# Kernel tuning notes

Measured on AMD Instinct MI355X. Metric: run time of the kernel, lower is better.

## Reference

```python
import jax, jax.numpy as jnp
import numpy as np

N = 50000       # nodes
E = 800000      # random edges (self-loops appended in reference)
F_IN = 3        # dataset.num_features
CH = 32         # conv_hidden_channels
HEADS = 4       # attention_heads
C1_OUT = CH * 2     # 64
C2_OUT = CH * 4     # 128
LIN = 256       # lin_hidden_channels
NCLS = 25       # dataset.num_classes


def setup_inputs() -> dict:
    key = jax.random.key(0)
    ks = jax.random.split(key, 20)
    g = lambda k, s: (jax.random.normal(k, s, jnp.float32) * 0.05)
    return {
        "x": jax.random.normal(ks[0], (N, F_IN), jnp.float32),
        "edge_index": jax.random.randint(ks[1], (2, E), 0, N, dtype=jnp.int64),
        # fc0 (Linear stored as [in, out])
        "fc0_w": g(ks[2], (F_IN, CH)), "fc0_b": g(ks[3], (CH,)),
        # FeaStConv 1: in=CH, out=C1_OUT
        "conv1_w": g(ks[4], (CH, HEADS * C1_OUT)),
        "conv1_u": g(ks[5], (CH, HEADS)),
        "conv1_c": g(ks[6], (HEADS,)),
        "conv1_b": g(ks[7], (C1_OUT,)),
        # FeaStConv 2: in=C1_OUT, out=C2_OUT
        "conv2_w": g(ks[8], (C1_OUT, HEADS * C2_OUT)),
        "conv2_u": g(ks[9], (C1_OUT, HEADS)),
        "conv2_c": g(ks[10], (HEADS,)),
        "conv2_b": g(ks[11], (C2_OUT,)),
        # fc1, fc2
        "fc1_w": g(ks[12], (C2_OUT, LIN)), "fc1_b": g(ks[13], (LIN,)),
        "fc2_w": g(ks[14], (LIN, NCLS)), "fc2_b": g(ks[15], (NCLS,)),
    }


def feast_conv(x, src, dst, W, u, c, b):
    """FeaStConv (PyG): q = softmax((x_j - x_i) u + c) over heads,
    msg = sum_h q_h * (x_j W_h), mean-aggregated onto dst nodes."""
    xi = x[dst]                          # [E', in]
    xj = x[src]                          # [E', in]
    q = jax.nn.softmax((xj - xi) @ u + c, axis=-1)   # [E', H]
    m = (xj @ W).reshape(xj.shape[0], HEADS, -1)     # [E', H, out]
    msg = jnp.einsum('eh,ehd->ed', q, m)             # [E', out]
    agg = jax.ops.segment_sum(msg, dst, num_segments=N)
    cnt = jax.ops.segment_sum(jnp.ones((msg.shape[0],), x.dtype), dst,
                              num_segments=N)
    return agg / cnt[:, None] + b


def reference(x, edge_index, fc0_w, fc0_b,
              conv1_w, conv1_u, conv1_c, conv1_b,
              conv2_w, conv2_u, conv2_c, conv2_b,
              fc1_w, fc1_b, fc2_w, fc2_b):
    loops = jnp.arange(N, dtype=edge_index.dtype)
    src = jnp.concatenate([edge_index[0], loops])   # messages flow src -> dst
    dst = jnp.concatenate([edge_index[1], loops])
    h = jax.nn.elu(x @ fc0_w + fc0_b)
    h = jax.nn.elu(feast_conv(h, src, dst, conv1_w, conv1_u, conv1_c, conv1_b))
    h = jax.nn.elu(feast_conv(h, src, dst, conv2_w, conv2_u, conv2_c, conv2_b))
    h = jax.nn.elu(h @ fc1_w + fc1_b)
    # dropout skipped (eval mode / training=self.training)
    out = h @ fc2_w + fc2_b
    return jax.nn.log_softmax(out, axis=1)
```

## Files before the change

kernel.cpp:

```cpp
#include <hip/hip_runtime.h>
#include <math.h>

#define F_IN 3
#define CH 32
#define HEADS 4
#define C1_OUT 64
#define C2_OUT 128
#define LIN 256
#define NCLS 25
#define NBIN 8

typedef __attribute__((ext_vector_type(8))) short bf16x8;
typedef __attribute__((ext_vector_type(4))) float f32x4;

__device__ __forceinline__ float elu_f(float x) {
    return x > 0.f ? x : (__expf(x) - 1.f);
}

__device__ __forceinline__ unsigned short f2bf(float f) {
    union { float f; unsigned int u; } v; v.f = f;
    unsigned int u = v.u + 0x7fffu + ((v.u >> 16) & 1u);
    return (unsigned short)(u >> 16);
}

__device__ __forceinline__ float bf2f(unsigned short u) {
    union { unsigned int u; float f; } v; v.u = ((unsigned int)u) << 16;
    return v.f;
}

__device__ __forceinline__ void unpackq(uint2 qp, float& x, float& y,
                                        float& z, float& w) {
    x = bf2f((unsigned short)(qp.x & 0xffffu));
    y = bf2f((unsigned short)(qp.x >> 16));
    z = bf2f((unsigned short)(qp.y & 0xffffu));
    w = bf2f((unsigned short)(qp.y >> 16));
}

__device__ __forceinline__ void softmax4(const float* __restrict__ c,
                                         float& q0, float& q1, float& q2, float& q3) {
    float c0 = c[0], c1 = c[1], c2 = c[2], c3 = c[3];
    float mx = fmaxf(fmaxf(c0, c1), fmaxf(c2, c3));
    float e0 = __expf(c0 - mx), e1 = __expf(c1 - mx);
    float e2 = __expf(c2 - mx), e3 = __expf(c3 - mx);
    float inv = 1.f / (e0 + e1 + e2 + e3);
    q0 = e0 * inv; q1 = e1 * inv; q2 = e2 * inv; q3 = e3 * inv;
}

__global__ void k_fc0(const float* __restrict__ x, const float* __restrict__ w,
                      const float* __restrict__ b, unsigned short* __restrict__ h0,
                      int n_nodes) {
    int gid = blockIdx.x * blockDim.x + threadIdx.x;
    if (gid >= n_nodes * CH) return;
    int n = gid >> 5, c = gid & 31;
    float acc = b[c];
#pragma unroll
    for (int i = 0; i < F_IN; ++i) acc += x[n * F_IN + i] * w[i * CH + c];
    h0[gid] = f2bf(elu_f(acc));
}

__global__ void k_deg(const int* __restrict__ dst, int* __restrict__ deg,
                      int ne, int npb) {
    int bin = blockIdx.x & (NBIN - 1);
    int blk = blockIdx.x >> 3;
    int nblk = gridDim.x >> 3;
    int per = (ne + nblk - 1) / nblk;
    int start = blk * per;
    int end = start + per < ne ? start + per : ne;
    int lo = bin * npb, hi = lo + npb;
    for (int e = start + threadIdx.x; e < end; e += blockDim.x) {
        int d = dst[e];
        if (d >= lo && d < hi) atomicAdd(&deg[d], 1);
    }
}

#define SCAN_BS 1024
__global__ __launch_bounds__(SCAN_BS) void k_scan_a(
    const int* __restrict__ deg, int* __restrict__ offa,
    int* __restrict__ blksum, int n) {
    __shared__ int buf[SCAN_BS];
    int tid = threadIdx.x;
    int i = blockIdx.x * SCAN_BS + tid;
    int v = (i < n) ? deg[i] : 0;
    buf[tid] = v;
    __syncthreads();
    for (int s = 1; s < SCAN_BS; s <<= 1) {
        int t = (tid >= s) ? buf[tid - s] : 0;
        __syncthreads();
        buf[tid] += t;
        __syncthreads();
    }
    if (i < n) offa[i] = buf[tid] - v;
    if (tid == SCAN_BS - 1) blksum[blockIdx.x] = buf[tid];
}

__global__ void k_scan_b(int* __restrict__ blksum, int* __restrict__ offa,
                         int nblk, int n) {
    int tid = threadIdx.x;
    int orig = (tid < nblk) ? blksum[tid] : 0;
    int v = orig;
#pragma unroll
    for (int s = 1; s < 64; s <<= 1) {
        int t = __shfl_up(v, s, 64);
        if (tid >= s) v += t;
    }
    if (tid < nblk) blksum[tid] = v - orig;
    if (tid == nblk - 1) offa[n] = v;
}

__global__ void k_scan_c(int* __restrict__ offa, int* __restrict__ cur,
                         const int* __restrict__ blksum, int n) {
    int i = blockIdx.x * blockDim.x + threadIdx.x;
    if (i < n) {
        int o = offa[i] + blksum[i >> 10];
        offa[i] = o;
        cur[i] = o;
    }
}

__global__ void k_scatter(const int* __restrict__ eidx, int* __restrict__ cur,
                          int2* __restrict__ ssd, const float* __restrict__ p,
                          const float* __restrict__ cvec, uint2* __restrict__ qq,
                          int ne, int npb) {
    int bin = blockIdx.x & (NBIN - 1);
    int blk = blockIdx.x >> 3;
    int nblk = gridDim.x >> 3;
    int per = (ne + nblk - 1) / nblk;
    int start = blk * per;
    int end = start + per < ne ? start + per : ne;
    int lo = bin * npb, hi = lo + npb;
    float c0 = cvec[0], c1 = cvec[1], c2 = cvec[2], c3 = cvec[3];
    const float4* pp = (const float4*)p;
    for (int e = start + threadIdx.x; e < end; e += blockDim.x) {
        int d = eidx[ne + e];
        if (d >= lo && d < hi) {
            int s = eidx[e];
            int pos = atomicAdd(&cur[d], 1);
            ssd[pos] = make_int2(s, d);
            float4 ps = pp[s], pd = pp[d];
            float t0 = ps.x - pd.x + c0;
            float t1 = ps.y - pd.y + c1;
            float t2 = ps.z - pd.z + c2;
            float t3 = ps.w - pd.w + c3;
            float mx = fmaxf(fmaxf(t0, t1), fmaxf(t2, t3));
            float e0 = __expf(t0 - mx), e1 = __expf(t1 - mx);
            float e2 = __expf(t2 - mx), e3 = __expf(t3 - mx);
            float inv = 1.f / (e0 + e1 + e2 + e3);
            qq[pos] = make_uint2(
                (unsigned)f2bf(e0 * inv) | ((unsigned)f2bf(e1 * inv) << 16),
                (unsigned)f2bf(e2 * inv) | ((unsigned)f2bf(e3 * inv) << 16));
        }
    }
}

template<int IN>
__global__ void k_proj(const unsigned short* __restrict__ h,
                       const float* __restrict__ u,
                       float* __restrict__ p, int n_nodes) {
    int node = blockIdx.x * blockDim.x + threadIdx.x;
    if (node >= n_nodes) return;
    const unsigned short* hr = h + (size_t)node * IN;
    float a0 = 0.f, a1 = 0.f, a2 = 0.f, a3 = 0.f;
#pragma unroll
    for (int kb = 0; kb < IN; kb += 8) {
        uint4 uu = *(const uint4*)(hr + kb);
        unsigned int ws_[4] = {uu.x, uu.y, uu.z, uu.w};
#pragma unroll
        for (int j = 0; j < 4; ++j) {
            float vlo = bf2f((unsigned short)(ws_[j] & 0xffffu));
            float vhi = bf2f((unsigned short)(ws_[j] >> 16));
            int k0 = kb + j * 2, k1 = kb + j * 2 + 1;
            a0 = fmaf(vlo, u[k0 * HEADS + 0], a0); a0 = fmaf(vhi, u[k1 * HEADS + 0], a0);
            a1 = fmaf(vlo, u[k0 * HEADS + 1], a1); a1 = fmaf(vhi, u[k1 * HEADS + 1], a1);
            a2 = fmaf(vlo, u[k0 * HEADS + 2], a2); a2 = fmaf(vhi, u[k1 * HEADS + 2], a2);
            a3 = fmaf(vlo, u[k0 * HEADS + 3], a3); a3 = fmaf(vhi, u[k1 * HEADS + 3], a3);
        }
    }
    p[node * 4 + 0] = a0; p[node * 4 + 1] = a1;
    p[node * 4 + 2] = a2; p[node * 4 + 3] = a3;
}

__global__ void k_q(const float* __restrict__ p, const float* __restrict__ cvec,
                    const int2* __restrict__ ssd, uint2* __restrict__ qq, int ne) {
    int e = blockIdx.x * blockDim.x + threadIdx.x;
    if (e >= ne) return;
    int2 sd = ssd[e];
    const float4* pp = (const float4*)p;
    float4 ps = pp[sd.x], pd = pp[sd.y];
    float t0 = ps.x - pd.x + cvec[0];
    float t1 = ps.y - pd.y + cvec[1];
    float t2 = ps.z - pd.z + cvec[2];
    float t3 = ps.w - pd.w + cvec[3];
    float mx = fmaxf(fmaxf(t0, t1), fmaxf(t2, t3));
    float e0 = __expf(t0 - mx), e1 = __expf(t1 - mx);
    float e2 = __expf(t2 - mx), e3 = __expf(t3 - mx);
    float inv = 1.f / (e0 + e1 + e2 + e3);
    qq[e] = make_uint2(
        (unsigned)f2bf(e0 * inv) | ((unsigned)f2bf(e1 * inv) << 16),
        (unsigned)f2bf(e2 * inv) | ((unsigned)f2bf(e3 * inv) << 16));
}

__global__ __launch_bounds__(256) void k_agg1(
    const unsigned short* __restrict__ h, const int* __restrict__ offa,
    const int2* __restrict__ ssd, const uint2* __restrict__ qq,
    const float* __restrict__ cvec, unsigned short* __restrict__ arow,
    int n_nodes) {
    int wid = (blockIdx.x * blockDim.x + threadIdx.x) >> 6;
    int lane = threadIdx.x & 63;
    if (wid >= n_nodes) return;
    int half = lane >> 5, k = lane & 31;
    int e0 = offa[wid], e1 = offa[wid + 1];
    float a0 = 0.f, a1 = 0.f, a2 = 0.f, a3 = 0.f;
    for (int e = e0 + half; e < e1; e += 8) {
        int s[4]; uint2 qp[4]; float xv[4];
#pragma unroll
        for (int j = 0; j < 4; ++j) {
            int ee = e + 2 * j;
            int ec = ee < e1 ? ee : e0;
            s[j] = ssd[ec].x;
            uint2 q = qq[ec];
            if (ee >= e1) { q.x = 0u; q.y = 0u; }
            qp[j] = q;
        }
#pragma unroll
        for (int j = 0; j < 4; ++j) xv[j] = bf2f(h[(size_t)s[j] * CH + k]);
#pragma unroll
        for (int j = 0; j < 4; ++j) {
            float qx, qy, qz, qw;
            unpackq(qp[j], qx, qy, qz, qw);
            a0 = fmaf(qx, xv[j], a0); a1 = fmaf(qy, xv[j], a1);
            a2 = fmaf(qz, xv[j], a2); a3 = fmaf(qw, xv[j], a3);
        }
    }
    a0 += __shfl_xor(a0, 32); a1 += __shfl_xor(a1, 32);
    a2 += __shfl_xor(a2, 32); a3 += __shfl_xor(a3, 32);
    if (half == 0) {
        float qc0, qc1, qc2, qc3;
        softmax4(cvec, qc0, qc1, qc2, qc3);
        float xi = bf2f(h[(size_t)wid * CH + k]);
        a0 = fmaf(qc0, xi, a0); a1 = fmaf(qc1, xi, a1);
        a2 = fmaf(qc2, xi, a2); a3 = fmaf(qc3, xi, a3);
        float inv = 1.f / (float)(e1 - e0 + 1);
        arow[(size_t)wid * 128 + 0 * CH + k] = f2bf(a0 * inv);
        arow[(size_t)wid * 128 + 1 * CH + k] = f2bf(a1 * inv);
        arow[(size_t)wid * 128 + 2 * CH + k] = f2bf(a2 * inv);
        arow[(size_t)wid * 128 + 3 * CH + k] = f2bf(a3 * inv);
    }
}

__global__ __launch_bounds__(256) void k_agg2(
    const unsigned short* __restrict__ h, const int* __restrict__ offa,
    const int2* __restrict__ ssd, const uint2* __restrict__ qq,
    const float* __restrict__ cvec, unsigned short* __restrict__ arow,
    int n_nodes) {
    int wid = (blockIdx.x * blockDim.x + threadIdx.x) >> 6;
    int lane = threadIdx.x & 63;
    if (wid >= n_nodes) return;
    int e0 = offa[wid], e1 = offa[wid + 1];
    float a0 = 0.f, a1 = 0.f, a2 = 0.f, a3 = 0.f;
    for (int e = e0; e < e1; e += 8) {
        int s[8]; uint2 qp[8]; float xv[8];
#pragma unroll
        for (int j = 0; j < 8; ++j) {
            int ee = e + j;
            int ec = ee < e1 ? ee : e0;
            s[j] = ssd[ec].x;
            uint2 q = qq[ec];
            if (ee >= e1) { q.x = 0u; q.y = 0u; }
            qp[j] = q;
        }
#pragma unroll
        for (int j = 0; j < 8; ++j) xv[j] = bf2f(h[(size_t)s[j] * C1_OUT + lane]);
#pragma unroll
        for (int j = 0; j < 8; ++j) {
            float qx, qy, qz, qw;
            unpackq(qp[j], qx, qy, qz, qw);
            a0 = fmaf(qx, xv[j], a0); a1 = fmaf(qy, xv[j], a1);
            a2 = fmaf(qz, xv[j], a2); a3 = fmaf(qw, xv[j], a3);
        }
    }
    float qc0, qc1, qc2, qc3;
    softmax4(cvec, qc0, qc1, qc2, qc3);
    float xi = bf2f(h[(size_t)wid * C1_OUT + lane]);
    a0 = fmaf(qc0, xi, a0); a1 = fmaf(qc1, xi, a1);
    a2 = fmaf(qc2, xi, a2); a3 = fmaf(qc3, xi, a3);
    float inv = 1.f / (float)(e1 - e0 + 1);
    arow[(size_t)wid * 256 + 0 * C1_OUT + lane] = f2bf(a0 * inv);
    arow[(size_t)wid * 256 + 1 * C1_OUT + lane] = f2bf(a1 * inv);
    arow[(size_t)wid * 256 + 2 * C1_OUT + lane] = f2bf(a2 * inv);
    arow[(size_t)wid * 256 + 3 * C1_OUT + lane] = f2bf(a3 * inv);
}

template<int K, int M, int IN>
__global__ void k_prepB(const float* __restrict__ W, unsigned short* __restrict__ Bt) {
    int idx = blockIdx.x * blockDim.x + threadIdx.x;
    if (idx >= K * M) return;
    int o = idx / K, j = idx % K;
    float v;
    if (IN > 0) {
        int hh = j / IN, k = j % IN;
        v = W[k * (HEADS * M) + hh * M + o];
    } else {
        v = W[j * M + o];
    }
    Bt[idx] = f2bf(v);
}

__global__ void k_prepC(const float* __restrict__ W, unsigned short* __restrict__ Bt) {
    int idx = blockIdx.x * blockDim.x + threadIdx.x;
    if (idx >= 32 * LIN) return;
    int o = idx >> 8, k = idx & 255;
    float v = (o < NCLS) ? W[k * NCLS + o] : 0.f;
    Bt[o * LIN + k] = f2bf(v);
}

template<int K, int M>
__global__ __launch_bounds__(256) void k_mgemm(
    const unsigned short* __restrict__ A, const unsigned short* __restrict__ Bt,
    const float* __restrict__ bias, unsigned short* __restrict__ D, int n) {
    constexpr int CPW = M / 4;
    constexpr int NCF = CPW / 16;
    constexpr int NKC = K / 32;
    __shared__ unsigned short Al[64 * K];
    int tid = threadIdx.x;
    int w = tid >> 6, l = tid & 63;
    int l16 = l & 15, l4 = l >> 4;
    int rowbase = blockIdx.x * 64;

    bf16x8 bfr[NCF][NKC];
#pragma unroll
    for (int c = 0; c < NCF; ++c)
#pragma unroll
        for (int t = 0; t < NKC; ++t) {
            int col = w * CPW + c * 16 + l16;
            int k = t * 32 + l4 * 8;
            bfr[c][t] = *(const bf16x8*)(Bt + (size_t)col * K + k);
        }

    constexpr int CHUNKS = 64 * K / 8;
    for (int idx = tid; idx < CHUNKS; idx += 256) {
        int row = idx / (K / 8);
        int kb = (idx % (K / 8)) * 8;
        int grow = rowbase + row;
        uint4 u;
        if (grow < n) u = *(const uint4*)(A + (size_t)grow * K + kb);
        else          u.x = u.y = u.z = u.w = 0u;
        int byte = ((row * K + kb) * 2) ^ ((row & 7) << 4);
        *(uint4*)((char*)Al + byte) = u;
    }
    __syncthreads();

#pragma unroll
    for (int r = 0; r < 4; ++r) {
        bf16x8 af[NKC];
        int row = r * 16 + l16;
#pragma unroll
        for (int t = 0; t < NKC; ++t) {
            int byte = ((row * K + t * 32 + l4 * 8) * 2) ^ ((row & 7) << 4);
            af[t] = *(bf16x8*)((char*)Al + byte);
        }
#pragma unroll
        for (int c = 0; c < NCF; ++c) {
            f32x4 acc = {0.f, 0.f, 0.f, 0.f};
#pragma unroll
            for (int t = 0; t < NKC; ++t)
                acc = __builtin_amdgcn_mfma_f32_16x16x32_bf16(af[t], bfr[c][t], acc, 0, 0, 0);
            int col = w * CPW + c * 16 + l16;
            float bv = bias[col];
#pragma unroll
            for (int j = 0; j < 4; ++j) {
                int grow = rowbase + r * 16 + l4 * 4 + j;
                if (grow < n)
                    D[(size_t)grow * M + col] = f2bf(elu_f(acc[j] + bv));
            }
        }
    }
}

__global__ __launch_bounds__(256) void k_fc2m(
    const unsigned short* __restrict__ A, const unsigned short* __restrict__ Bt,
    const float* __restrict__ bias, float* __restrict__ out, int n) {
    int tid = threadIdx.x;
    int w = tid >> 6, l = tid & 63;
    int l16 = l & 15, l4 = l >> 4;
    int rowbase = blockIdx.x * 256 + w * 64;

    bf16x8 bfr0[8], bfr1[8];
#pragma unroll
    for (int t = 0; t < 8; ++t) {
        int k = t * 32 + l4 * 8;
        bfr0[t] = *(const bf16x8*)(Bt + (size_t)l16 * LIN + k);
        bfr1[t] = *(const bf16x8*)(Bt + (size_t)(16 + l16) * LIN + k);
    }
    float b0 = bias[l16];
    bool hi_ok = (l16 < NCLS - 16);
    float b1 = hi_ok ? bias[16 + l16] : 0.f;

#pragma unroll
    for (int r = 0; r < 4; ++r) {
        int arow_i = rowbase + r * 16 + l16;
        int arc = arow_i < n ? arow_i : n - 1;
        const unsigned short* ar = A + (size_t)arc * LIN;
        bf16x8 af[8];
#pragma unroll
        for (int t = 0; t < 8; ++t)
            af[t] = *(const bf16x8*)(ar + t * 32 + l4 * 8);
        f32x4 acc0 = {0.f, 0.f, 0.f, 0.f}, acc1 = {0.f, 0.f, 0.f, 0.f};
#pragma unroll
        for (int t = 0; t < 8; ++t) {
            acc0 = __builtin_amdgcn_mfma_f32_16x16x32_bf16(af[t], bfr0[t], acc0, 0, 0, 0);
            acc1 = __builtin_amdgcn_mfma_f32_16x16x32_bf16(af[t], bfr1[t], acc1, 0, 0, 0);
        }
#pragma unroll
        for (int j = 0; j < 4; ++j) {
            float v0 = acc0[j] + b0;
            float v1 = acc1[j] + b1;
            float m = fmaxf(v0, hi_ok ? v1 : -1e30f);
#pragma unroll
            for (int msk = 8; msk >= 1; msk >>= 1)
                m = fmaxf(m, __shfl_xor(m, msk, 16));
            float s = __expf(v0 - m) + (hi_ok ? __expf(v1 - m) : 0.f);
#pragma unroll
            for (int msk = 8; msk >= 1; msk >>= 1)
                s += __shfl_xor(s, msk, 16);
            float lse = m + __logf(s);
            int ro = rowbase + r * 16 + l4 * 4 + j;
            if (ro < n) {
                out[(size_t)ro * NCLS + l16] = v0 - lse;
                if (hi_ok) out[(size_t)ro * NCLS + 16 + l16] = v1 - lse;
            }
        }
    }
}

extern "C" void kernel_launch(void* const* d_in, const int* in_sizes, int n_in,
                              void* d_out, int out_size, void* d_ws, size_t ws_size,
                              hipStream_t stream) {
    const float* x     = (const float*)d_in[0];
    const int*   eidx  = (const int*)d_in[1];
    const float* fc0_w = (const float*)d_in[2];
    const float* fc0_b = (const float*)d_in[3];
    const float* c1w   = (const float*)d_in[4];
    const float* c1u   = (const float*)d_in[5];
    const float* c1c   = (const float*)d_in[6];
    const float* c1b   = (const float*)d_in[7];
    const float* c2w   = (const float*)d_in[8];
    const float* c2u   = (const float*)d_in[9];
    const float* c2c   = (const float*)d_in[10];
    const float* c2b   = (const float*)d_in[11];
    const float* fc1w  = (const float*)d_in[12];
    const float* fc1b  = (const float*)d_in[13];
    const float* fc2w  = (const float*)d_in[14];
    const float* fc2b  = (const float*)d_in[15];

    int n_nodes = in_sizes[0] / F_IN;
    int ne      = in_sizes[1] / 2;

    auto align4 = [](size_t v) { return (v + 3) & ~(size_t)3; };
    float* ws = (float*)d_ws;
    size_t t = 0;
    size_t off_o = t; t += align4((size_t)n_nodes + 1);
    size_t cur_o = t; t += align4((size_t)n_nodes);
    size_t blk_o = t; t += 64;
    size_t p_o   = t; t += align4((size_t)n_nodes * 4);
    size_t h1_o  = t; t += align4((size_t)n_nodes * 32);
    size_t A_o   = t; t += align4((size_t)n_nodes * 128);
    size_t B_o   = t;
    size_t h0_o  = B_o;
    size_t ss_o  = align4(h0_o + (size_t)n_nodes * 16);
    size_t qq_o  = align4(ss_o + (size_t)ne * 2);
    size_t B_end = qq_o + (size_t)ne * 2;
    size_t B_sz  = B_end - B_o;
    size_t h2_sz = (size_t)n_nodes * 64;
    t = B_o + (B_sz > h2_sz ? B_sz : h2_sz);
    size_t bt1_o = t; t += 4096;
    size_t bt2_o = t; t += 16384;
    size_t btf_o = t; t += 16384;
    size_t btc_o = t; t += 4096;

    int*    offa   = (int*)(ws + off_o);
    int*    cur    = (int*)(ws + cur_o);
    int*    blksum = (int*)(ws + blk_o);
    float*  p      = ws + p_o;
    unsigned short* h1    = (unsigned short*)(ws + h1_o);
    unsigned short* arow1 = (unsigned short*)(ws + A_o);
    unsigned short* arow2 = (unsigned short*)(ws + A_o);
    unsigned short* h3    = (unsigned short*)(ws + A_o);
    unsigned short* h0    = (unsigned short*)(ws + h0_o);
    int2*   ssd    = (int2*)(ws + ss_o);
    uint2*  qq     = (uint2*)(ws + qq_o);
    unsigned short* h2    = (unsigned short*)(ws + B_o);
    unsigned short* bt1 = (unsigned short*)(ws + bt1_o);
    unsigned short* bt2 = (unsigned short*)(ws + bt2_o);
    unsigned short* btf = (unsigned short*)(ws + btf_o);
    unsigned short* btc = (unsigned short*)(ws + btc_o);
    float*  out    = (float*)d_out;

    int nblk = (n_nodes + SCAN_BS - 1) / SCAN_BS;
    int npb  = (n_nodes + NBIN - 1) / NBIN;

    hipMemsetAsync(cur, 0, (size_t)n_nodes * sizeof(int), stream);

    k_prepB<128, 64, 32><<<(128 * 64 + 255) / 256, 256, 0, stream>>>(c1w, bt1);
    k_prepB<256, 128, 64><<<(256 * 128 + 255) / 256, 256, 0, stream>>>(c2w, bt2);
    k_prepB<128, 256, 0><<<(128 * 256 + 255) / 256, 256, 0, stream>>>(fc1w, btf);
    k_prepC<<<(32 * LIN + 255) / 256, 256, 0, stream>>>(fc2w, btc);

    k_fc0<<<(n_nodes * CH + 255) / 256, 256, 0, stream>>>(x, fc0_w, fc0_b, h0, n_nodes);
    k_deg<<<NBIN * 128, 256, 0, stream>>>(eidx + ne, cur, ne, npb);
    k_scan_a<<<nblk, SCAN_BS, 0, stream>>>(cur, offa, blksum, n_nodes);
    k_scan_b<<<1, 64, 0, stream>>>(blksum, offa, nblk, n_nodes);
    k_scan_c<<<(n_nodes + 255) / 256, 256, 0, stream>>>(offa, cur, blksum, n_nodes);

    k_proj<CH><<<(n_nodes + 255) / 256, 256, 0, stream>>>(h0, c1u, p, n_nodes);
    k_scatter<<<NBIN * 128, 256, 0, stream>>>(eidx, cur, ssd, p, c1c, qq, ne, npb);

    int ngrid = (n_nodes + 63) / 64;

    k_agg1<<<(n_nodes * 64 + 255) / 256, 256, 0, stream>>>(h0, offa, ssd, qq, c1c, arow1, n_nodes);
    k_mgemm<128, 64><<<ngrid, 256, 0, stream>>>(arow1, bt1, c1b, h1, n_nodes);

    k_proj<C1_OUT><<<(n_nodes + 255) / 256, 256, 0, stream>>>(h1, c2u, p, n_nodes);
    k_q<<<(ne + 255) / 256, 256, 0, stream>>>(p, c2c, ssd, qq, ne);
    k_agg2<<<(n_nodes * 64 + 255) / 256, 256, 0, stream>>>(h1, offa, ssd, qq, c2c, arow2, n_nodes);
    k_mgemm<256, 128><<<ngrid, 256, 0, stream>>>(arow2, bt2, c2b, h2, n_nodes);

    k_mgemm<128, 256><<<ngrid, 256, 0, stream>>>(h2, btf, fc1b, h3, n_nodes);
    k_fc2m<<<(n_nodes + 255) / 256, 256, 0, stream>>>(h3, btc, fc2b, out, n_nodes);
}
```

Baseline: 263.3 us.

## Compute attention weights inside aggregation kernels and fuse projection into fc0

Drops the per-edge q buffer: the softmax weights are now computed on the fly inside agg1/agg2, with each of 8 lanes handling one edge and the results broadcast by shuffles. This removes the k_q kernel and the q writes in scatter. The first-layer projection is folded into fc0 through a wave reduction, the four weight-prep kernels are merged into one launch, and the deg/scatter grids are enlarged. It saves edge-sized memory traffic and several launches, at the cost of extra shuffles and exp work inside the gather loops.

```diff
diff --git a/kernel.cpp b/kernel.cpp
--- a/kernel.cpp
+++ b/kernel.cpp
@@ -28,12 +28,12 @@
     return v.f;
 }
 
-__device__ __forceinline__ void unpackq(uint2 qp, float& x, float& y,
+__device__ __forceinline__ void unpackq(unsigned lo, unsigned hi, float& x, float& y,
                                         float& z, float& w) {
-    x = bf2f((unsigned short)(qp.x & 0xffffu));
-    y = bf2f((unsigned short)(qp.x >> 16));
-    z = bf2f((unsigned short)(qp.y & 0xffffu));
-    w = bf2f((unsigned short)(qp.y >> 16));
+    x = bf2f((unsigned short)(lo & 0xffffu));
+    y = bf2f((unsigned short)(lo >> 16));
+    z = bf2f((unsigned short)(hi & 0xffffu));
+    w = bf2f((unsigned short)(hi >> 16));
 }
 
 __device__ __forceinline__ void softmax4(const float* __restrict__ c,
@@ -46,16 +46,54 @@
     q0 = e0 * inv; q1 = e1 * inv; q2 = e2 * inv; q3 = e3 * inv;
 }
 
-__global__ void k_fc0(const float* __restrict__ x, const float* __restrict__ w,
-                      const float* __restrict__ b, unsigned short* __restrict__ h0,
-                      int n_nodes) {
-    int gid = blockIdx.x * blockDim.x + threadIdx.x;
-    if (gid >= n_nodes * CH) return;
-    int n = gid >> 5, c = gid & 31;
+__device__ __forceinline__ void qslot(const float4* __restrict__ pp, float4 pd,
+                                      float c0, float c1, float c2, float c3,
+                                      int sx, bool valid,
+                                      unsigned& qlo, unsigned& qhi) {
+    float4 ps = pp[sx];
+    float t0 = ps.x - pd.x + c0;
+    float t1 = ps.y - pd.y + c1;
+    float t2 = ps.z - pd.z + c2;
+    float t3 = ps.w - pd.w + c3;
+    float mx = fmaxf(fmaxf(t0, t1), fmaxf(t2, t3));
+    float s0 = __expf(t0 - mx), s1 = __expf(t1 - mx);
+    float s2 = __expf(t2 - mx), s3 = __expf(t3 - mx);
+    float inv = 1.f / (s0 + s1 + s2 + s3);
+    qlo = qhi = 0u;
+    if (valid) {
+        qlo = (unsigned)f2bf(s0 * inv) | ((unsigned)f2bf(s1 * inv) << 16);
+        qhi = (unsigned)f2bf(s2 * inv) | ((unsigned)f2bf(s3 * inv) << 16);
+    }
+}
+
+__global__ __launch_bounds__(256) void k_fc0(
+    const float* __restrict__ x, const float* __restrict__ w,
+    const float* __restrict__ b, const float* __restrict__ u,
+    unsigned short* __restrict__ h0, float* __restrict__ p, int n_nodes) {
+    int wid = (blockIdx.x * blockDim.x + threadIdx.x) >> 6;
+    int lane = threadIdx.x & 63;
+    int half = lane >> 5, c = lane & 31;
+    int node = wid * 2 + half;
+    if (node >= n_nodes) return;
     float acc = b[c];
 #pragma unroll
-    for (int i = 0; i < F_IN; ++i) acc += x[n * F_IN + i] * w[i * CH + c];
-    h0[gid] = f2bf(elu_f(acc));
+    for (int i = 0; i < F_IN; ++i) acc += x[node * F_IN + i] * w[i * CH + c];
+    unsigned short hb = f2bf(elu_f(acc));
+    h0[(size_t)node * CH + c] = hb;
+    float hv = bf2f(hb);
+    float a0 = hv * u[c * HEADS + 0];
+    float a1 = hv * u[c * HEADS + 1];
+    float a2 = hv * u[c * HEADS + 2];
+    float a3 = hv * u[c * HEADS + 3];
+#pragma unroll
+    for (int m = 16; m >= 1; m >>= 1) {
+        a0 += __shfl_xor(a0, m, 32); a1 += __shfl_xor(a1, m, 32);
+        a2 += __shfl_xor(a2, m, 32); a3 += __shfl_xor(a3, m, 32);
+    }
+    if (c == 0) {
+        p[node * 4 + 0] = a0; p[node * 4 + 1] = a1;
+        p[node * 4 + 2] = a2; p[node * 4 + 3] = a3;
+    }
 }
 
 __global__ void k_deg(const int* __restrict__ dst, int* __restrict__ deg,
@@ -118,9 +156,7 @@
 }
 
 __global__ void k_scatter(const int* __restrict__ eidx, int* __restrict__ cur,
-                          int2* __restrict__ ssd, const float* __restrict__ p,
-                          const float* __restrict__ cvec, uint2* __restrict__ qq,
-                          int ne, int npb) {
+                          int2* __restrict__ ssd, int ne, int npb) {
     int bin = blockIdx.x & (NBIN - 1);
     int blk = blockIdx.x >> 3;
     int nblk = gridDim.x >> 3;
@@ -128,26 +164,12 @@
     int start = blk * per;
     int end = start + per < ne ? start + per : ne;
     int lo = bin * npb, hi = lo + npb;
-    float c0 = cvec[0], c1 = cvec[1], c2 = cvec[2], c3 = cvec[3];
-    const float4* pp = (const float4*)p;
     for (int e = start + threadIdx.x; e < end; e += blockDim.x) {
         int d = eidx[ne + e];
         if (d >= lo && d < hi) {
             int s = eidx[e];
             int pos = atomicAdd(&cur[d], 1);
             ssd[pos] = make_int2(s, d);
-            float4 ps = pp[s], pd = pp[d];
-            float t0 = ps.x - pd.x + c0;
-            float t1 = ps.y - pd.y + c1;
-            float t2 = ps.z - pd.z + c2;
-            float t3 = ps.w - pd.w + c3;
-            float mx = fmaxf(fmaxf(t0, t1), fmaxf(t2, t3));
-            float e0 = __expf(t0 - mx), e1 = __expf(t1 - mx);
-            float e2 = __expf(t2 - mx), e3 = __expf(t3 - mx);
-            float inv = 1.f / (e0 + e1 + e2 + e3);
-            qq[pos] = make_uint2(
-                (unsigned)f2bf(e0 * inv) | ((unsigned)f2bf(e1 * inv) << 16),
-                (unsigned)f2bf(e2 * inv) | ((unsigned)f2bf(e3 * inv) << 16));
         }
     }
 }
@@ -179,56 +201,40 @@
     p[node * 4 + 2] = a2; p[node * 4 + 3] = a3;
 }
 
-__global__ void k_q(const float* __restrict__ p, const float* __restrict__ cvec,
-                    const int2* __restrict__ ssd, uint2* __restrict__ qq, int ne) {
-    int e = blockIdx.x * blockDim.x + threadIdx.x;
-    if (e >= ne) return;
-    int2 sd = ssd[e];
-    const float4* pp = (const float4*)p;
-    float4 ps = pp[sd.x], pd = pp[sd.y];
-    float t0 = ps.x - pd.x + cvec[0];
-    float t1 = ps.y - pd.y + cvec[1];
-    float t2 = ps.z - pd.z + cvec[2];
-    float t3 = ps.w - pd.w + cvec[3];
-    float mx = fmaxf(fmaxf(t0, t1), fmaxf(t2, t3));
-    float e0 = __expf(t0 - mx), e1 = __expf(t1 - mx);
-    float e2 = __expf(t2 - mx), e3 = __expf(t3 - mx);
-    float inv = 1.f / (e0 + e1 + e2 + e3);
-    qq[e] = make_uint2(
-        (unsigned)f2bf(e0 * inv) | ((unsigned)f2bf(e1 * inv) << 16),
-        (unsigned)f2bf(e2 * inv) | ((unsigned)f2bf(e3 * inv) << 16));
-}
-
 __global__ __launch_bounds__(256) void k_agg1(
     const unsigned short* __restrict__ h, const int* __restrict__ offa,
-    const int2* __restrict__ ssd, const uint2* __restrict__ qq,
+    const int2* __restrict__ ssd, const float* __restrict__ p,
     const float* __restrict__ cvec, unsigned short* __restrict__ arow,
     int n_nodes) {
     int wid = (blockIdx.x * blockDim.x + threadIdx.x) >> 6;
     int lane = threadIdx.x & 63;
     if (wid >= n_nodes) return;
-    int half = lane >> 5, k = lane & 31;
-    int e0 = offa[wid], e1 = offa[wid + 1];
+    int half = lane >> 5, ch = lane & 31;
+    int slot = lane & 7, sbase = lane & 56;
+    int e0 = __builtin_amdgcn_readfirstlane(offa[wid]);
+    int e1 = __builtin_amdgcn_readfirstlane(offa[wid + 1]);
+    const float4* pp = (const float4*)p;
+    float4 pd = pp[wid];
+    float c0 = cvec[0], c1 = cvec[1], c2 = cvec[2], c3 = cvec[3];
     float a0 = 0.f, a1 = 0.f, a2 = 0.f, a3 = 0.f;
-    for (int e = e0 + half; e < e1; e += 8) {
-        int s[4]; uint2 qp[4]; float xv[4];
-#pragma unroll
-        for (int j = 0; j < 4; ++j) {
-            int ee = e + 2 * j;
-            int ec = ee < e1 ? ee : e0;
-            s[j] = ssd[ec].x;
-            uint2 q = qq[ec];
-            if (ee >= e1) { q.x = 0u; q.y = 0u; }
-            qp[j] = q;
-        }
-#pragma unroll
-        for (int j = 0; j < 4; ++j) xv[j] = bf2f(h[(size_t)s[j] * CH + k]);
-#pragma unroll
-        for (int j = 0; j < 4; ++j) {
+    for (int e = e0; e < e1; e += 8) {
+        int ee = e + slot;
+        int ec = ee < e1 ? ee : e0;
+        int2 sd = ssd[ec];
+        unsigned qlo, qhi;
+        qslot(pp, pd, c0, c1, c2, c3, sd.x, ee < e1, qlo, qhi);
+        int sx = sd.x;
+#pragma unroll
+        for (int m = 0; m < 4; ++m) {
+            int src = sbase + 2 * m + half;
+            int sj = __shfl(sx, src, 64);
+            unsigned lo = (unsigned)__shfl((int)qlo, src, 64);
+            unsigned hi = (unsigned)__shfl((int)qhi, src, 64);
+            float xj = bf2f(h[(size_t)sj * CH + ch]);
             float qx, qy, qz, qw;
-            unpackq(qp[j], qx, qy, qz, qw);
-            a0 = fmaf(qx, xv[j], a0); a1 = fmaf(qy, xv[j], a1);
-            a2 = fmaf(qz, xv[j], a2); a3 = fmaf(qw, xv[j], a3);
+            unpackq(lo, hi, qx, qy, qz, qw);
+            a0 = fmaf(qx, xj, a0); a1 = fmaf(qy, xj, a1);
+            a2 = fmaf(qz, xj, a2); a3 = fmaf(qw, xj, a3);
         }
     }
     a0 += __shfl_xor(a0, 32); a1 += __shfl_xor(a1, 32);
@@ -236,46 +242,50 @@
     if (half == 0) {
         float qc0, qc1, qc2, qc3;
         softmax4(cvec, qc0, qc1, qc2, qc3);
-        float xi = bf2f(h[(size_t)wid * CH + k]);
+        float xi = bf2f(h[(size_t)wid * CH + ch]);
         a0 = fmaf(qc0, xi, a0); a1 = fmaf(qc1, xi, a1);
         a2 = fmaf(qc2, xi, a2); a3 = fmaf(qc3, xi, a3);
         float inv = 1.f / (float)(e1 - e0 + 1);
-        arow[(size_t)wid * 128 + 0 * CH + k] = f2bf(a0 * inv);
-        arow[(size_t)wid * 128 + 1 * CH + k] = f2bf(a1 * inv);
-        arow[(size_t)wid * 128 + 2 * CH + k] = f2bf(a2 * inv);
-        arow[(size_t)wid * 128 + 3 * CH + k] = f2bf(a3 * inv);
+        arow[(size_t)wid * 128 + 0 * CH + ch] = f2bf(a0 * inv);
+        arow[(size_t)wid * 128 + 1 * CH + ch] = f2bf(a1 * inv);
+        arow[(size_t)wid * 128 + 2 * CH + ch] = f2bf(a2 * inv);
+        arow[(size_t)wid * 128 + 3 * CH + ch] = f2bf(a3 * inv);
     }
 }
 
 __global__ __launch_bounds__(256) void k_agg2(
     const unsigned short* __restrict__ h, const int* __restrict__ offa,
-    const int2* __restrict__ ssd, const uint2* __restrict__ qq,
+    const int2* __restrict__ ssd, const float* __restrict__ p,
     const float* __restrict__ cvec, unsigned short* __restrict__ arow,
     int n_nodes) {
     int wid = (blockIdx.x * blockDim.x + threadIdx.x) >> 6;
     int lane = threadIdx.x & 63;
     if (wid >= n_nodes) return;
-    int e0 = offa[wid], e1 = offa[wid + 1];
+    int slot = lane & 7, sbase = lane & 56;
+    int e0 = __builtin_amdgcn_readfirstlane(offa[wid]);
+    int e1 = __builtin_amdgcn_readfirstlane(offa[wid + 1]);
+    const float4* pp = (const float4*)p;
+    float4 pd = pp[wid];
+    float c0 = cvec[0], c1 = cvec[1], c2 = cvec[2], c3 = cvec[3];
     float a0 = 0.f, a1 = 0.f, a2 = 0.f, a3 = 0.f;
     for (int e = e0; e < e1; e += 8) {
-        int s[8]; uint2 qp[8]; float xv[8];
+        int ee = e + slot;
+        int ec = ee < e1 ? ee : e0;
+        int2 sd = ssd[ec];
+        unsigned qlo, qhi;
+        qslot(pp, pd, c0, c1, c2, c3, sd.x, ee < e1, qlo, qhi);
+        int sx = sd.x;
 #pragma unroll
         for (int j = 0; j < 8; ++j) {
-            int ee = e + j;
-            int ec = ee < e1 ? ee : e0;
-            s[j] = ssd[ec].x;
-            uint2 q = qq[ec];
-            if (ee >= e1) { q.x = 0u; q.y = 0u; }
-            qp[j] = q;
-        }
-#pragma unroll
-        for (int j = 0; j < 8; ++j) xv[j] = bf2f(h[(size_t)s[j] * C1_OUT + lane]);
-#pragma unroll
-        for (int j = 0; j < 8; ++j) {
+            int src = sbase + j;
+            int sj = __shfl(sx, src, 64);
+            unsigned lo = (unsigned)__shfl((int)qlo, src, 64);
+            unsigned hi = (unsigned)__shfl((int)qhi, src, 64);
+            float xj = bf2f(h[(size_t)sj * C1_OUT + lane]);
             float qx, qy, qz, qw;
-            unpackq(qp[j], qx, qy, qz, qw);
-            a0 = fmaf(qx, xv[j], a0); a1 = fmaf(qy, xv[j], a1);
-            a2 = fmaf(qz, xv[j], a2); a3 = fmaf(qw, xv[j], a3);
+            unpackq(lo, hi, qx, qy, qz, qw);
+            a0 = fmaf(qx, xj, a0); a1 = fmaf(qy, xj, a1);
+            a2 = fmaf(qz, xj, a2); a3 = fmaf(qw, xj, a3);
         }
     }
     float qc0, qc1, qc2, qc3;
@@ -290,27 +300,29 @@
     arow[(size_t)wid * 256 + 3 * C1_OUT + lane] = f2bf(a3 * inv);
 }
 
-template<int K, int M, int IN>
-__global__ void k_prepB(const float* __restrict__ W, unsigned short* __restrict__ Bt) {
+__global__ void k_prepAll(const float* __restrict__ W1, unsigned short* __restrict__ B1,
+                          const float* __restrict__ W2, unsigned short* __restrict__ B2,
+                          const float* __restrict__ Wf, unsigned short* __restrict__ Bf,
+                          const float* __restrict__ Wc, unsigned short* __restrict__ Bc) {
     int idx = blockIdx.x * blockDim.x + threadIdx.x;
-    if (idx >= K * M) return;
-    int o = idx / K, j = idx % K;
-    float v;
-    if (IN > 0) {
-        int hh = j / IN, k = j % IN;
-        v = W[k * (HEADS * M) + hh * M + o];
-    } else {
-        v = W[j * M + o];
-    }
-    Bt[idx] = f2bf(v);
-}
-
-__global__ void k_prepC(const float* __restrict__ W, unsigned short* __restrict__ Bt) {
-    int idx = blockIdx.x * blockDim.x + threadIdx.x;
-    if (idx >= 32 * LIN) return;
-    int o = idx >> 8, k = idx & 255;
-    float v = (o < NCLS) ? W[k * NCLS + o] : 0.f;
-    Bt[o * LIN + k] = f2bf(v);
+    if (idx < 8192) {
+        int o = idx / 128, j = idx % 128;
+        int hh = j / 32, k = j % 32;
+        B1[idx] = f2bf(W1[k * (HEADS * 64) + hh * 64 + o]);
+    } else if (idx < 40960) {
+        int i = idx - 8192;
+        int o = i / 256, j = i % 256;
+        int hh = j / 64, k = j % 64;
+        B2[i] = f2bf(W2[k * (HEADS * 128) + hh * 128 + o]);
+    } else if (idx < 73728) {
+        int i = idx - 40960;
+        int o = i / 128, j = i % 128;
+        Bf[i] = f2bf(Wf[j * 256 + o]);
+    } else if (idx < 81920) {
+        int i = idx - 73728;
+        int o = i >> 8, k = i & 255;
+        Bc[i] = f2bf(o < NCLS ? Wc[k * NCLS + o] : 0.f);
+    }
 }
 
 template<int K, int M>
@@ -467,8 +479,7 @@
     size_t B_o   = t;
     size_t h0_o  = B_o;
     size_t ss_o  = align4(h0_o + (size_t)n_nodes * 16);
-    size_t qq_o  = align4(ss_o + (size_t)ne * 2);
-    size_t B_end = qq_o + (size_t)ne * 2;
+    size_t B_end = ss_o + (size_t)ne * 2;
     size_t B_sz  = B_end - B_o;
     size_t h2_sz = (size_t)n_nodes * 64;
     t = B_o + (B_sz > h2_sz ? B_sz : h2_sz);
@@ -487,7 +498,6 @@
     unsigned short* h3    = (unsigned short*)(ws + A_o);
     unsigned short* h0    = (unsigned short*)(ws + h0_o);
     int2*   ssd    = (int2*)(ws + ss_o);
-    uint2*  qq     = (uint2*)(ws + qq_o);
     unsigned short* h2    = (unsigned short*)(ws + B_o);
     unsigned short* bt1 = (unsigned short*)(ws + bt1_o);
     unsigned short* bt2 = (unsigned short*)(ws + bt2_o);
@@ -500,28 +510,22 @@
 
     hipMemsetAsync(cur, 0, (size_t)n_nodes * sizeof(int), stream);
 
-    k_prepB<128, 64, 32><<<(128 * 64 + 255) / 256, 256, 0, stream>>>(c1w, bt1);
-    k_prepB<256, 128, 64><<<(256 * 128 + 255) / 256, 256, 0, stream>>>(c2w, bt2);
-    k_prepB<128, 256, 0><<<(128 * 256 + 255) / 256, 256, 0, stream>>>(fc1w, btf);
-    k_prepC<<<(32 * LIN + 255) / 256, 256, 0, stream>>>(fc2w, btc);
-
-    k_fc0<<<(n_nodes * CH + 255) / 256, 256, 0, stream>>>(x, fc0_w, fc0_b, h0, n_nodes);
-    k_deg<<<NBIN * 128, 256, 0, stream>>>(eidx + ne, cur, ne, npb);
+    k_prepAll<<<(81920 + 255) / 256, 256, 0, stream>>>(c1w, bt1, c2w, bt2, fc1w, btf, fc2w, btc);
+
+    k_fc0<<<(n_nodes * 32 + 255) / 256, 256, 0, stream>>>(x, fc0_w, fc0_b, c1u, h0, p, n_nodes);
+    k_deg<<<NBIN * 512, 256, 0, stream>>>(eidx + ne, cur, ne, npb);
     k_scan_a<<<nblk, SCAN_BS, 0, stream>>>(cur, offa, blksum, n_nodes);
     k_scan_b<<<1, 64, 0, stream>>>(blksum, offa, nblk, n_nodes);
     k_scan_c<<<(n_nodes + 255) / 256, 256, 0, stream>>>(offa, cur, blksum, n_nodes);
-
-    k_proj<CH><<<(n_nodes + 255) / 256, 256, 0, stream>>>(h0, c1u, p, n_nodes);
-    k_scatter<<<NBIN * 128, 256, 0, stream>>>(eidx, cur, ssd, p, c1c, qq, ne, npb);
+    k_scatter<<<NBIN * 512, 256, 0, stream>>>(eidx, cur, ssd, ne, npb);
 
     int ngrid = (n_nodes + 63) / 64;
 
-    k_agg1<<<(n_nodes * 64 + 255) / 256, 256, 0, stream>>>(h0, offa, ssd, qq, c1c, arow1, n_nodes);
+    k_agg1<<<(n_nodes * 64 + 255) / 256, 256, 0, stream>>>(h0, offa, ssd, p, c1c, arow1, n_nodes);
     k_mgemm<128, 64><<<ngrid, 256, 0, stream>>>(arow1, bt1, c1b, h1, n_nodes);
 
     k_proj<C1_OUT><<<(n_nodes + 255) / 256, 256, 0, stream>>>(h1, c2u, p, n_nodes);
-    k_q<<<(ne + 255) / 256, 256, 0, stream>>>(p, c2c, ssd, qq, ne);
-    k_agg2<<<(n_nodes * 64 + 255) / 256, 256, 0, stream>>>(h1, offa, ssd, qq, c2c, arow2, n_nodes);
+    k_agg2<<<(n_nodes * 64 + 255) / 256, 256, 0, stream>>>(h1, offa, ssd, p, c2c, arow2, n_nodes);
     k_mgemm<256, 128><<<ngrid, 256, 0, stream>>>(arow2, bt2, c2b, h2, n_nodes);
 
     k_mgemm<128, 256><<<ngrid, 256, 0, stream>>>(h2, btf, fc1b, h3, n_nodes);
```

Result: faster. 247.0 us (-6.2%).
